# Performance work log

Measured on AMD Instinct MI355X. Metric: run time of the kernel, lower is better.

The kernel has to match this reference:

```python
import jax, jax.numpy as jnp
import numpy as np

D, H, WIN, TEMP = 512, 8, 2, 1.0
DH = D // H
SCALE = DH ** -0.5
SHIFT = WIN // 2


def _ln(x, g, b):
    m = jnp.mean(x, -1, keepdims=True)
    v = jnp.mean(jnp.square(x - m), -1, keepdims=True)
    return (x - m) * jax.lax.rsqrt(v + 1e-5) * g + b


def _win_attn(q, k, v):
    a = jax.nn.softmax(jnp.einsum('nhqd,nhkd->nhqk', q * SCALE, k) / TEMP, axis=-1)
    return jnp.einsum('nhqk,nhkd->nhqd', a, v)


def _self_block(x, p):
    qkv_w, qkv_b, proj_w, proj_b, n1g, n1b, n2g, n2b = p
    b, t, d = x.shape
    sc = x
    xw = _ln(x, n1g, n1b).reshape(b * t // WIN, WIN, d)  # window partition
    qkv = (xw @ qkv_w + qkv_b).reshape(-1, WIN, 3, H, DH).transpose(2, 0, 3, 1, 4)
    o = _win_attn(qkv[0], qkv[1], qkv[2])
    o = o.transpose(0, 2, 1, 3).reshape(-1, WIN, d) @ proj_w + proj_b
    return _ln(o.reshape(b, t, d) + sc, n2g, n2b)  # window reverse + residual


def _self_tf(x, p):
    x = _self_block(x, p)
    x = jnp.roll(x, -SHIFT, axis=1)   # sequence_shift
    x = _self_block(x, p)
    return jnp.roll(x, SHIFT, axis=1)  # sequence_inverse_shift


def _cross_block(x, y, p):
    q_w, q_b, kv_w, kv_b, proj_w, proj_b, n1g, n1b, n2g, n2b = p
    b, t, d = x.shape
    sc = x
    xw = _ln(x, n1g, n1b).reshape(-1, WIN, d)
    yw = _ln(y, n1g, n1b).reshape(-1, WIN, d)  # shared pre_norm, as in source
    q = (xw @ q_w + q_b).reshape(-1, WIN, H, DH).transpose(0, 2, 1, 3)
    kv = (yw @ kv_w + kv_b).reshape(-1, WIN, 2, H, DH).transpose(2, 0, 3, 1, 4)
    o = _win_attn(q, kv[0], kv[1])
    o = o.transpose(0, 2, 1, 3).reshape(-1, WIN, d) @ proj_w + proj_b
    return _ln(o.reshape(b, t, d) + sc, n2g, n2b)


def _cross_tf(x, y, p):
    x = _cross_block(x, y, p)
    x = jnp.roll(x, -SHIFT, axis=1)
    x = _cross_block(x, jnp.roll(y, -SHIFT, axis=1), p)
    return jnp.roll(x, SHIFT, axis=1)


def setup_inputs() -> dict:
    key = jax.random.key(0)
    ks = iter(jax.random.split(key, 40))
    B, T = 16, 4096
    d = {
        'x': jax.random.normal(next(ks), (B, T, D), jnp.float32),
        'y': jax.random.normal(next(ks), (B, T, D), jnp.float32),
    }

    def w(shape):
        return jax.random.normal(next(ks), shape, jnp.float32) * 0.02

    for m in ('wa', 'wv'):  # within-modal audio / video
        d[m + '_qkv_w'] = w((D, 3 * D)); d[m + '_qkv_b'] = jnp.zeros((3 * D,), jnp.float32)
        d[m + '_proj_w'] = w((D, D));    d[m + '_proj_b'] = jnp.zeros((D,), jnp.float32)
        d[m + '_n1_g'] = jnp.ones((D,), jnp.float32); d[m + '_n1_b'] = jnp.zeros((D,), jnp.float32)
        d[m + '_n2_g'] = jnp.ones((D,), jnp.float32); d[m + '_n2_b'] = jnp.zeros((D,), jnp.float32)
    # shared cross-modal transformer
    d['cm_q_w'] = w((D, D));      d['cm_q_b'] = jnp.zeros((D,), jnp.float32)
    d['cm_kv_w'] = w((D, 2 * D)); d['cm_kv_b'] = jnp.zeros((2 * D,), jnp.float32)
    d['cm_proj_w'] = w((D, D));   d['cm_proj_b'] = jnp.zeros((D,), jnp.float32)
    d['cm_n1_g'] = jnp.ones((D,), jnp.float32); d['cm_n1_b'] = jnp.zeros((D,), jnp.float32)
    d['cm_n2_g'] = jnp.ones((D,), jnp.float32); d['cm_n2_b'] = jnp.zeros((D,), jnp.float32)
    return d


def reference(x, y,
              wa_qkv_w, wa_qkv_b, wa_proj_w, wa_proj_b, wa_n1_g, wa_n1_b, wa_n2_g, wa_n2_b,
              wv_qkv_w, wv_qkv_b, wv_proj_w, wv_proj_b, wv_n1_g, wv_n1_b, wv_n2_g, wv_n2_b,
              cm_q_w, cm_q_b, cm_kv_w, cm_kv_b, cm_proj_w, cm_proj_b, cm_n1_g, cm_n1_b, cm_n2_g, cm_n2_b):
    pa = (wa_qkv_w, wa_qkv_b, wa_proj_w, wa_proj_b, wa_n1_g, wa_n1_b, wa_n2_g, wa_n2_b)
    pv = (wv_qkv_w, wv_qkv_b, wv_proj_w, wv_proj_b, wv_n1_g, wv_n1_b, wv_n2_g, wv_n2_b)
    pc = (cm_q_w, cm_q_b, cm_kv_w, cm_kv_b, cm_proj_w, cm_proj_b, cm_n1_g, cm_n1_b, cm_n2_g, cm_n2_b)
    # args.s1_attn == 'all' path
    x = _self_tf(x, pa)
    y = _self_tf(y, pv)
    xc = _cross_tf(x, y, pc)
    yc = _cross_tf(y, x, pc)
    return jnp.stack([x + xc, y + yc])  # (2, B, T, D)
```

## Files before the change

### kernel.cpp

```cpp
#include <hip/hip_runtime.h>

typedef unsigned short u16;
typedef unsigned int u32;
typedef __attribute__((ext_vector_type(8))) short short8;
typedef __attribute__((ext_vector_type(4))) short short4v;
typedef __attribute__((ext_vector_type(4))) float f32x4;

#define D_MODEL 512
#define NH 8
#define TSEQ 4096
#define NB 16
#define NROWS (NB*TSEQ)
#define QK_SCALE 0.125f
#define KDIM 512
#define NKI (KDIM/32)

__device__ __forceinline__ float b2f(u16 u){
    union { float f; unsigned int i; } v; v.i = ((unsigned int)u) << 16; return v.f;
}
__device__ __forceinline__ u16 f2b(float f){
    union { float f; unsigned int i; } v; v.f = f;
    unsigned int r = v.i + 0x7FFFu + ((v.i >> 16) & 1u);
    return (u16)(r >> 16);
}

__device__ __forceinline__ void async_copy16(u16* lds, const u16* g){
    __builtin_amdgcn_global_load_lds(
        (const __attribute__((address_space(1))) u32*)g,
        (__attribute__((address_space(3))) u32*)lds, 16, 0, 0);
}

__global__ void wconv_kernel(const float* __restrict__ W, u16* __restrict__ Wt, int K, int N){
    int idx = blockIdx.x * 256 + threadIdx.x;
    if (idx >= K * N) return;
    int n = idx / K;
    int k = idx - n * K;
    Wt[idx] = f2b(W[(size_t)k * N + n]);
}

__global__ __launch_bounds__(256) void ln_kernel(
    const float* __restrict__ X, const float* __restrict__ g,
    const float* __restrict__ b, u16* __restrict__ out)
{
    int row  = blockIdx.x * 4 + (threadIdx.x >> 6);
    int lane = threadIdx.x & 63;
    size_t base = (size_t)row * D_MODEL + lane * 8;
    float4 x0 = *(const float4*)(X + base);
    float4 x1 = *(const float4*)(X + base + 4);
    float t[8] = {x0.x,x0.y,x0.z,x0.w,x1.x,x1.y,x1.z,x1.w};
    float s = 0.f, ss = 0.f;
    #pragma unroll
    for (int j = 0; j < 8; j++){ s += t[j]; ss += t[j]*t[j]; }
    #pragma unroll
    for (int m = 1; m < 64; m <<= 1){ s += __shfl_xor(s, m); ss += __shfl_xor(ss, m); }
    float mean = s * (1.f/D_MODEL);
    float var  = ss * (1.f/D_MODEL) - mean*mean;
    float rst  = rsqrtf(var + 1e-5f);
    float4 g0 = *(const float4*)(g + lane*8);
    float4 g1 = *(const float4*)(g + lane*8 + 4);
    float4 c0 = *(const float4*)(b + lane*8);
    float4 c1 = *(const float4*)(b + lane*8 + 4);
    float gv[8] = {g0.x,g0.y,g0.z,g0.w,g1.x,g1.y,g1.z,g1.w};
    float bv[8] = {c0.x,c0.y,c0.z,c0.w,c1.x,c1.y,c1.z,c1.w};
    short8 o;
    #pragma unroll
    for (int j = 0; j < 8; j++) o[j] = (short)f2b((t[j]-mean)*rst*gv[j] + bv[j]);
    *(short8*)(out + base) = o;
}

template<int XINBF, int OUTBF>
__global__ __launch_bounds__(256) void resln_kernel(
    const u16* __restrict__ P, const void* __restrict__ Xin,
    const u16* __restrict__ Add,
    const float* __restrict__ g, const float* __restrict__ b,
    void* __restrict__ out,
    u16* __restrict__ lnout, const float* __restrict__ g2, const float* __restrict__ b2)
{
    int row  = blockIdx.x * 4 + (threadIdx.x >> 6);
    int lane = threadIdx.x & 63;
    size_t base = (size_t)row * D_MODEL + lane * 8;
    short8 pv = *(const short8*)(P + base);
    float t[8];
    if constexpr (XINBF){
        short8 xv = *(const short8*)((const u16*)Xin + base);
        #pragma unroll
        for (int j = 0; j < 8; j++) t[j] = b2f((u16)pv[j]) + b2f((u16)xv[j]);
    } else {
        float4 x0 = *(const float4*)((const float*)Xin + base);
        float4 x1 = *(const float4*)((const float*)Xin + base + 4);
        float xr[8] = {x0.x,x0.y,x0.z,x0.w,x1.x,x1.y,x1.z,x1.w};
        #pragma unroll
        for (int j = 0; j < 8; j++) t[j] = b2f((u16)pv[j]) + xr[j];
    }
    float s = 0.f, ss = 0.f;
    #pragma unroll
    for (int j = 0; j < 8; j++){ s += t[j]; ss += t[j]*t[j]; }
    #pragma unroll
    for (int m = 1; m < 64; m <<= 1){ s += __shfl_xor(s, m); ss += __shfl_xor(ss, m); }
    float mean = s * (1.f/D_MODEL);
    float var  = ss * (1.f/D_MODEL) - mean*mean;
    float rst  = rsqrtf(var + 1e-5f);
    float4 g0 = *(const float4*)(g + lane*8);
    float4 g1 = *(const float4*)(g + lane*8 + 4);
    float4 c0 = *(const float4*)(b + lane*8);
    float4 c1 = *(const float4*)(b + lane*8 + 4);
    float gv[8] = {g0.x,g0.y,g0.z,g0.w,g1.x,g1.y,g1.z,g1.w};
    float bv[8] = {c0.x,c0.y,c0.z,c0.w,c1.x,c1.y,c1.z,c1.w};
    float o[8];
    #pragma unroll
    for (int j = 0; j < 8; j++) o[j] = (t[j]-mean)*rst*gv[j] + bv[j];

    if (lnout){
        float s2 = 0.f, ss2 = 0.f;
        #pragma unroll
        for (int j = 0; j < 8; j++){ s2 += o[j]; ss2 += o[j]*o[j]; }
        #pragma unroll
        for (int m = 1; m < 64; m <<= 1){ s2 += __shfl_xor(s2, m); ss2 += __shfl_xor(ss2, m); }
        float mean2 = s2 * (1.f/D_MODEL);
        float var2  = ss2 * (1.f/D_MODEL) - mean2*mean2;
        float rst2  = rsqrtf(var2 + 1e-5f);
        float4 g20 = *(const float4*)(g2 + lane*8);
        float4 g21 = *(const float4*)(g2 + lane*8 + 4);
        float4 b20 = *(const float4*)(b2 + lane*8);
        float4 b21 = *(const float4*)(b2 + lane*8 + 4);
        float g2v[8] = {g20.x,g20.y,g20.z,g20.w,g21.x,g21.y,g21.z,g21.w};
        float b2v[8] = {b20.x,b20.y,b20.z,b20.w,b21.x,b21.y,b21.z,b21.w};
        short8 lo;
        #pragma unroll
        for (int j = 0; j < 8; j++) lo[j] = (short)f2b((o[j]-mean2)*rst2*g2v[j] + b2v[j]);
        *(short8*)(lnout + base) = lo;
    }
    if (Add){
        short8 av = *(const short8*)(Add + base);
        #pragma unroll
        for (int j = 0; j < 8; j++) o[j] += b2f((u16)av[j]);
    }
    if constexpr (OUTBF){
        short8 ov;
        #pragma unroll
        for (int j = 0; j < 8; j++) ov[j] = (short)f2b(o[j]);
        *(short8*)((u16*)out + base) = ov;
    } else {
        float4 r0 = {o[0],o[1],o[2],o[3]};
        float4 r1 = {o[4],o[5],o[6],o[7]};
        *(float4*)((float*)out + base)     = r0;
        *(float4*)((float*)out + base + 4) = r1;
    }
}

__global__ __launch_bounds__(256) void qkvattn_kernel(
    const u16* __restrict__ A, const u16* __restrict__ Wt,
    const float* __restrict__ bias, u16* __restrict__ O, int shift)
{
    __shared__ __align__(16) u16 lds[2][20*512];
    int tid  = threadIdx.x;
    int lane = tid & 63;
    int wid  = tid >> 6;

    int bid  = blockIdx.x;
    int swz  = (bid & 7) * 512 + (bid >> 3);
    int head = swz >> 9;
    int rt   = swz & 511;
    int bt   = rt >> 5;
    int tb   = (rt & 31) * 128;

    f32x4 acc[2][12];
    f32x4 zero = {0.f,0.f,0.f,0.f};
    #pragma unroll
    for (int m = 0; m < 2; m++)
        #pragma unroll
        for (int n = 0; n < 12; n++) acc[m][n] = zero;

    int rr = lane >> 2, kc = (lane & 3) * 8;
    const u16* p[5];
    int cidb = wid * 5;
    #pragma unroll
    for (int q = 0; q < 5; q++){
        int cid = cidb + q;
        if (cid < 8){
            int i   = cid*16 + rr;
            int tok = (tb + shift + i) & (TSEQ-1);
            p[q] = A + ((size_t)bt * TSEQ + tok) * KDIM + kc;
        } else {
            int cb   = cid - 8;
            int wrow = (cb >> 2) * 512 + head*64 + (cb & 3)*16 + rr;
            p[q] = Wt + (size_t)wrow * KDIM + kc;
        }
    }

    int lrow = lane & 15;
    int lk   = (lane >> 4) * 8;
    int aoff = (wid*32 + lrow) * 32 + lk;
    int boff = 8*512 + lrow*32 + lk;

    #pragma unroll
    for (int q = 0; q < 5; q++){ async_copy16(&lds[0][(cidb+q)*512], p[q]); p[q] += 32; }
    asm volatile("s_waitcnt vmcnt(0)" ::: "memory");
    __syncthreads();

    #pragma unroll
    for (int t = 0; t < NKI; t++){
        const u16* cbuf = lds[t & 1];
        u16* nbuf = (u16*)lds[(t & 1) ^ 1];
        if (t < NKI-1){
            #pragma unroll
            for (int q = 0; q < 5; q++){ async_copy16(&nbuf[(cidb+q)*512], p[q]); p[q] += 32; }
        }
        short8 af[2], bf[12];
        #pragma unroll
        for (int m = 0; m < 2; m++) af[m] = *(const short8*)(cbuf + aoff + m*512);
        #pragma unroll
        for (int n = 0; n < 12; n++) bf[n] = *(const short8*)(cbuf + boff + n*512);
        #pragma unroll
        for (int m = 0; m < 2; m++)
            #pragma unroll
            for (int n = 0; n < 12; n++)
                acc[m][n] = __builtin_amdgcn_mfma_f32_16x16x32_bf16(af[m], bf[n], acc[m][n], 0, 0, 0);
        if (t < NKI-1){
            asm volatile("s_waitcnt vmcnt(0)" ::: "memory");
            __syncthreads();
        }
    }

    int g_ = lane >> 4, lc = lane & 15;
    float bq[4], bk[4], bv[4];
    #pragma unroll
    for (int n = 0; n < 4; n++){
        int d = head*64 + n*16 + lc;
        bq[n] = bias[d]; bk[n] = bias[512 + d]; bv[n] = bias[1024 + d];
    }
    #pragma unroll
    for (int m = 0; m < 2; m++){
        #pragma unroll
        for (int wnd = 0; wnd < 2; wnd++){
            int ja = 2*wnd, jb = ja + 1;
            float s00=0.f, s01=0.f, s10=0.f, s11=0.f;
            #pragma unroll
            for (int n = 0; n < 4; n++){
                float qa = acc[m][n][ja] + bq[n],  qb = acc[m][n][jb] + bq[n];
                float ka = acc[m][4+n][ja] + bk[n], kb = acc[m][4+n][jb] + bk[n];
                s00 += qa*ka; s01 += qa*kb; s10 += qb*ka; s11 += qb*kb;
            }
            #pragma unroll
            for (int msk = 1; msk < 16; msk <<= 1){
                s00 += __shfl_xor(s00, msk); s01 += __shfl_xor(s01, msk);
                s10 += __shfl_xor(s10, msk); s11 += __shfl_xor(s11, msk);
            }
            s00 *= QK_SCALE; s01 *= QK_SCALE; s10 *= QK_SCALE; s11 *= QK_SCALE;
            float m0 = fmaxf(s00, s01), m1 = fmaxf(s10, s11);
            float e00 = expf(s00-m0), e01 = expf(s01-m0);
            float e10 = expf(s10-m1), e11 = expf(s11-m1);
            float ia = 1.f/(e00+e01), ib = 1.f/(e10+e11);
            float a00 = e00*ia, a01 = e01*ia, a10 = e10*ib, a11 = e11*ib;
            int ra = wid*32 + m*16 + 4*g_ + ja;
            int ta = (tb + shift + ra) & (TSEQ-1);
            size_t growa = (size_t)bt * TSEQ + ta;
            size_t growb = (size_t)bt * TSEQ + ((ta + 1) & (TSEQ-1));
            #pragma unroll
            for (int n = 0; n < 4; n++){
                float va = acc[m][8+n][ja] + bv[n], vb = acc[m][8+n][jb] + bv[n];
                int col = head*64 + n*16 + lc;
                O[growa * D_MODEL + col] = f2b(a00*va + a01*vb);
                O[growb * D_MODEL + col] = f2b(a10*va + a11*vb);
            }
        }
    }
}

#define AOFc(buf,h) (((buf)*2+(h))*8192)
#define BOFc(buf,h) (32768 + ((buf)*2+(h))*8192)

__global__ __launch_bounds__(512, 2) void gemm256_kernel(
    const u16* __restrict__ A, const u16* __restrict__ Wt,
    const float* __restrict__ bias, u16* __restrict__ C, int N, int nN)
{
    __shared__ __align__(16) u16 sh[65536];
    u16* sh_ = (u16*)sh;
    const int tid = threadIdx.x, lane = tid & 63, wid = tid >> 6;
    const int wm = wid >> 2, wn = wid & 3;
    const int cpx = (int)gridDim.x >> 3;
    const int swz = ((int)blockIdx.x & 7) * cpx + ((int)blockIdx.x >> 3);
    const int row0 = (swz / nN) * 256;
    const int col0 = (swz % nN) * 256;

    f32x4 acc[8][4];
    f32x4 zero = {0.f,0.f,0.f,0.f};
    #pragma unroll
    for (int m = 0; m < 8; m++)
        #pragma unroll
        for (int n = 0; n < 4; n++) acc[m][n] = zero;

    const int lrow = lane & 15, khi = lane >> 4;
    const int swx   = (lrow & 4) << 2;
    const int kcol0 = (khi*8) ^ swx;
    const int kcol1 = (32 + khi*8) ^ swx;
    const int aR0 = AOFc(0, wm) , aR1 = AOFc(1, wm);
    const int bh  = wn >> 1;
    const int bR0 = BOFc(0, bh), bR1 = BOFc(1, bh);
    const int abase = lrow*64;
    const int bbase = (wn & 1)*4096 + lrow*64;

    const u16* Ag = A  + (size_t)row0 * KDIM;
    const u16* Bg = Wt + (size_t)col0 * KDIM;
    const int csrc = ((lane & 7) * 8) ^ (((lane >> 3) & 4) << 2);
    const int srow = wid*16 + (lane >> 3);

    short8 af[4][2], bf[4][2];

    #define STG(dstOff, gp) { \
        const u16* s1_ = (gp) + (size_t)srow*KDIM + csrc; \
        u16* d1_ = sh_ + (dstOff) + wid*1024; \
        async_copy16(d1_, s1_); \
        async_copy16(d1_ + 512, s1_ + (size_t)8*KDIM); }
    #define RDA(bufR, h) { \
        const u16* p_ = sh_ + (bufR) + abase; \
        _Pragma("unroll") \
        for (int i_ = 0; i_ < 4; i_++){ \
            af[i_][0] = *(const short8*)(p_ + ((h)*4+i_)*1024 + kcol0); \
            af[i_][1] = *(const short8*)(p_ + ((h)*4+i_)*1024 + kcol1); } }
    #define RDB(bufR, nh) { \
        const u16* p_ = sh_ + (bufR) + bbase; \
        _Pragma("unroll") \
        for (int j_ = 0; j_ < 2; j_++){ \
            bf[(nh)*2+j_][0] = *(const short8*)(p_ + ((nh)*2+j_)*1024 + kcol0); \
            bf[(nh)*2+j_][1] = *(const short8*)(p_ + ((nh)*2+j_)*1024 + kcol1); } }
    #define MM(mh, nh) { \
        __builtin_amdgcn_s_setprio(1); \
        _Pragma("unroll") \
        for (int m_ = 0; m_ < 4; m_++) \
            _Pragma("unroll") \
            for (int n_ = 0; n_ < 2; n_++){ \
                acc[(mh)*4+m_][(nh)*2+n_] = __builtin_amdgcn_mfma_f32_16x16x32_bf16(af[m_][0], bf[(nh)*2+n_][0], acc[(mh)*4+m_][(nh)*2+n_], 0,0,0); \
                acc[(mh)*4+m_][(nh)*2+n_] = __builtin_amdgcn_mfma_f32_16x16x32_bf16(af[m_][1], bf[(nh)*2+n_][1], acc[(mh)*4+m_][(nh)*2+n_], 0,0,0); } \
        __builtin_amdgcn_s_setprio(0); }
    #define BAR() { asm volatile("" ::: "memory"); __builtin_amdgcn_s_barrier(); asm volatile("" ::: "memory"); }
    #define VMW4() asm volatile("s_waitcnt vmcnt(4)" ::: "memory")
    #define VMW0() asm volatile("s_waitcnt vmcnt(0)" ::: "memory")

    STG(BOFc(0,0), Bg);
    STG(BOFc(0,1), Bg + (size_t)128*KDIM);
    STG(AOFc(0,0), Ag);
    STG(AOFc(0,1), Ag + (size_t)128*KDIM);
    STG(BOFc(1,0), Bg + 64);
    STG(BOFc(1,1), Bg + (size_t)128*KDIM + 64);
    VMW4();
    BAR();

    #pragma unroll
    for (int i = 0; i < 4; i++){
        RDA(aR0, 0); RDB(bR0, 0);
        STG(AOFc(1,0), Ag + (2*i+1)*64);
        BAR(); MM(0,0); BAR();

        RDB(bR0, 1);
        STG(AOFc(1,1), Ag + (size_t)128*KDIM + (2*i+1)*64);
        BAR(); MM(0,1); BAR();

        RDA(aR0, 1);
        if (i < 3) STG(BOFc(0,0), Bg + (2*i+2)*64);
        BAR(); MM(1,0); BAR();

        if (i < 3){ STG(BOFc(0,1), Bg + (size_t)128*KDIM + (2*i+2)*64); VMW4(); }
        else      { VMW0(); }
        BAR(); MM(1,1); BAR();

        RDA(aR1, 0); RDB(bR1, 0);
        if (i < 3) STG(AOFc(0,0), Ag + (2*i+2)*64);
        BAR(); MM(0,0); BAR();

        RDB(bR1, 1);
        if (i < 3) STG(AOFc(0,1), Ag + (size_t)128*KDIM + (2*i+2)*64);
        BAR(); MM(0,1); BAR();

        RDA(aR1, 1);
        if (i < 3) STG(BOFc(1,0), Bg + (2*i+3)*64);
        BAR(); MM(1,0); BAR();

        if (i < 3){ STG(BOFc(1,1), Bg + (size_t)128*KDIM + (2*i+3)*64); VMW4(); }
        BAR(); MM(1,1); BAR();
    }

    int g_ = lane >> 4, lc = lane & 15;
    #pragma unroll
    for (int n = 0; n < 4; n++){
        int c = col0 + wn*64 + n*16 + lc;
        float bvv = bias[c];
        #pragma unroll
        for (int m = 0; m < 8; m++){
            int r = row0 + wm*128 + m*16 + 4*g_;
            f32x4 v = acc[m][n];
            C[(size_t)(r+0) * N + c] = f2b(v[0] + bvv);
            C[(size_t)(r+1) * N + c] = f2b(v[1] + bvv);
            C[(size_t)(r+2) * N + c] = f2b(v[2] + bvv);
            C[(size_t)(r+3) * N + c] = f2b(v[3] + bvv);
        }
    }
    #undef STG
    #undef RDA
    #undef RDB
    #undef MM
    #undef BAR
    #undef VMW4
    #undef VMW0
}

__global__ __launch_bounds__(256) void attn_cross_kernel(
    const u16* __restrict__ Q, const u16* __restrict__ KV,
    u16* __restrict__ O, int shift)
{
    int tsk  = blockIdx.x * 4 + (threadIdx.x >> 6);
    int lane = threadIdx.x & 63;
    int w  = tsk >> 1;
    int hb = tsk & 1;
    int bt = w >> 11;
    int wt = w & 2047;
    int t0 = (2*wt + shift) & (TSEQ - 1);
    int t1 = (t0 + 1) & (TSEQ - 1);
    size_t g0 = (size_t)bt * TSEQ + t0;
    size_t g1 = (size_t)bt * TSEQ + t1;
    int col = hb*256 + lane*4;
    short4v q0 = *(const short4v*)(Q  + g0*512  + col);
    short4v q1 = *(const short4v*)(Q  + g1*512  + col);
    short4v k0 = *(const short4v*)(KV + g0*1024 + col);
    short4v k1 = *(const short4v*)(KV + g1*1024 + col);
    short4v v0 = *(const short4v*)(KV + g0*1024 + 512 + col);
    short4v v1 = *(const short4v*)(KV + g1*1024 + 512 + col);
    float s00=0.f, s01=0.f, s10=0.f, s11=0.f;
    float v0f[4], v1f[4];
    #pragma unroll
    for (int j = 0; j < 4; j++){
        float qa = b2f((u16)q0[j]), qb = b2f((u16)q1[j]);
        float ka = b2f((u16)k0[j]), kb = b2f((u16)k1[j]);
        v0f[j] = b2f((u16)v0[j]); v1f[j] = b2f((u16)v1[j]);
        s00 += qa*ka; s01 += qa*kb; s10 += qb*ka; s11 += qb*kb;
    }
    #pragma unroll
    for (int m = 1; m < 16; m <<= 1){
        s00 += __shfl_xor(s00, m); s01 += __shfl_xor(s01, m);
        s10 += __shfl_xor(s10, m); s11 += __shfl_xor(s11, m);
    }
    s00 *= QK_SCALE; s01 *= QK_SCALE; s10 *= QK_SCALE; s11 *= QK_SCALE;
    float m0 = fmaxf(s00, s01), m1 = fmaxf(s10, s11);
    float e00 = expf(s00 - m0), e01 = expf(s01 - m0);
    float e10 = expf(s10 - m1), e11 = expf(s11 - m1);
    float ia = 1.f/(e00 + e01), ib = 1.f/(e10 + e11);
    float a00 = e00*ia, a01 = e01*ia, a10 = e10*ib, a11 = e11*ib;
    short4v o0, o1;
    #pragma unroll
    for (int j = 0; j < 4; j++){
        o0[j] = (short)f2b(a00*v0f[j] + a01*v1f[j]);
        o1[j] = (short)f2b(a10*v0f[j] + a11*v1f[j]);
    }
    *(short4v*)(O + g0*512 + col) = o0;
    *(short4v*)(O + g1*512 + col) = o1;
}

extern "C" void kernel_launch(void* const* d_in, const int* in_sizes, int n_in,
                              void* d_out, int out_size, void* d_ws, size_t ws_size,
                              hipStream_t stream)
{
    const float* x = (const float*)d_in[0];
    const float* y = (const float*)d_in[1];
    const float* wa_qkv_w = (const float*)d_in[2];  const float* wa_qkv_b = (const float*)d_in[3];
    const float* wa_proj_w= (const float*)d_in[4];  const float* wa_proj_b= (const float*)d_in[5];
    const float* wa_n1g   = (const float*)d_in[6];  const float* wa_n1b   = (const float*)d_in[7];
    const float* wa_n2g   = (const float*)d_in[8];  const float* wa_n2b   = (const float*)d_in[9];
    const float* wv_qkv_w = (const float*)d_in[10]; const float* wv_qkv_b = (const float*)d_in[11];
    const float* wv_proj_w= (const float*)d_in[12]; const float* wv_proj_b= (const float*)d_in[13];
    const float* wv_n1g   = (const float*)d_in[14]; const float* wv_n1b   = (const float*)d_in[15];
    const float* wv_n2g   = (const float*)d_in[16]; const float* wv_n2b   = (const float*)d_in[17];
    const float* cm_q_w   = (const float*)d_in[18]; const float* cm_q_b   = (const float*)d_in[19];
    const float* cm_kv_w  = (const float*)d_in[20]; const float* cm_kv_b  = (const float*)d_in[21];
    const float* cm_proj_w= (const float*)d_in[22]; const float* cm_proj_b= (const float*)d_in[23];
    const float* cm_n1g   = (const float*)d_in[24]; const float* cm_n1b   = (const float*)d_in[25];
    const float* cm_n2g   = (const float*)d_in[26]; const float* cm_n2b   = (const float*)d_in[27];

    char* ws = (char*)d_ws;
    const size_t SZ_B16 = (size_t)NROWS * D_MODEL * 2;
    u16* F1b = (u16*)(ws);
    u16* XFb = (u16*)(ws + 1*SZ_B16);
    u16* YFb = (u16*)(ws + 2*SZ_B16);
    u16* XN  = (u16*)(ws + 3*SZ_B16);
    u16* CN  = (u16*)(ws + 4*SZ_B16);
    u16* XLN = (u16*)(ws + 5*SZ_B16);
    u16* YLN = (u16*)(ws + 6*SZ_B16);
    u16* O   = (u16*)(ws + 7*SZ_B16);
    u16* KVb = (u16*)(ws + 8*SZ_B16);
    u16* WB  = (u16*)(ws + 10*SZ_B16);

    u16* PB = KVb;

    u16* wa_qkv_t  = WB;
    u16* wa_proj_t = wa_qkv_t  + 1536*512;
    u16* wv_qkv_t  = wa_proj_t + 512*512;
    u16* wv_proj_t = wv_qkv_t  + 1536*512;
    u16* cm_q_t    = wv_proj_t + 512*512;
    u16* cm_kv_t   = cm_q_t    + 512*512;
    u16* cm_proj_t = cm_kv_t   + 1024*512;

    auto conv = [&](const float* W, u16* Wt, int K, int N){
        int total = K * N;
        wconv_kernel<<<(total + 255) / 256, 256, 0, stream>>>(W, Wt, K, N);
    };
    conv(wa_qkv_w,  wa_qkv_t,  512, 1536);
    conv(wa_proj_w, wa_proj_t, 512, 512);
    conv(wv_qkv_w,  wv_qkv_t,  512, 1536);
    conv(wv_proj_w, wv_proj_t, 512, 512);
    conv(cm_q_w,    cm_q_t,    512, 512);
    conv(cm_kv_w,   cm_kv_t,   512, 1024);
    conv(cm_proj_w, cm_proj_t, 512, 512);

    const int lnGrid   = NROWS / 4;
    const int attnGrid = NROWS / 2 * 2 / 4;
    const int qaGrid   = (NROWS / 128) * NH;

    auto gemm = [&](const u16* Ain, const u16* Wt, const float* bias, u16* Cout, int N){
        int nN = N / 256;
        gemm256_kernel<<<(NROWS/256) * nN, 512, 0, stream>>>(Ain, Wt, bias, Cout, N, nN);
    };

    auto self_chain = [&](const float* in, u16* outFb, u16* outLN,
                          const u16* qkvT, const float* qkv_b,
                          const u16* projT, const float* proj_b,
                          const float* n1g, const float* n1b,
                          const float* n2g, const float* n2b){
        ln_kernel<<<lnGrid, 256, 0, stream>>>(in, n1g, n1b, XN);
        qkvattn_kernel<<<qaGrid, 256, 0, stream>>>(XN, qkvT, qkv_b, O, 0);
        gemm(O, projT, proj_b, PB, 512);
        resln_kernel<0,1><<<lnGrid, 256, 0, stream>>>(PB, in, nullptr, n2g, n2b, F1b, XN, n1g, n1b);
        qkvattn_kernel<<<qaGrid, 256, 0, stream>>>(XN, qkvT, qkv_b, O, 1);
        gemm(O, projT, proj_b, PB, 512);
        resln_kernel<1,1><<<lnGrid, 256, 0, stream>>>(PB, F1b, nullptr, n2g, n2b, outFb, outLN, cm_n1g, cm_n1b);
    };

    self_chain(x, XFb, XLN, wa_qkv_t, wa_qkv_b, wa_proj_t, wa_proj_b, wa_n1g, wa_n1b, wa_n2g, wa_n2b);
    self_chain(y, YFb, YLN, wv_qkv_t, wv_qkv_b, wv_proj_t, wv_proj_b, wv_n1g, wv_n1b, wv_n2g, wv_n2b);

    float* out0 = (float*)d_out;
    float* out1 = out0 + (size_t)NROWS * D_MODEL;

    auto cross_chain = [&](const u16* qLN, const u16* kvLN, const u16* resFb, float* outF){
        gemm(kvLN, cm_kv_t, cm_kv_b, KVb, 1024);
        gemm(qLN,  cm_q_t,  cm_q_b,  XN,  512);
        attn_cross_kernel<<<attnGrid, 256, 0, stream>>>(XN, KVb, O, 0);
        gemm(O, cm_proj_t, cm_proj_b, XN, 512);
        resln_kernel<1,1><<<lnGrid, 256, 0, stream>>>(XN, resFb, nullptr, cm_n2g, cm_n2b, F1b, CN, cm_n1g, cm_n1b);
        gemm(CN, cm_q_t, cm_q_b, XN, 512);
        attn_cross_kernel<<<attnGrid, 256, 0, stream>>>(XN, KVb, O, 1);
        gemm(O, cm_proj_t, cm_proj_b, XN, 512);
        resln_kernel<1,0><<<lnGrid, 256, 0, stream>>>(XN, F1b, resFb, cm_n2g, cm_n2b, outF, nullptr, nullptr, nullptr);
    };

    cross_chain(XLN, YLN, XFb, out0);
    cross_chain(YLN, XLN, YFb, out1);
}
```

Measured before the change: 2.144 ms.

## Batch x and y streams into single launches over concatenated rows

```diff
diff --git a/kernel.cpp b/kernel.cpp
--- a/kernel.cpp
+++ b/kernel.cpp
@@ -11,6 +11,7 @@
 #define TSEQ 4096
 #define NB 16
 #define NROWS (NB*TSEQ)
+#define M2 (2*NROWS)
 #define QK_SCALE 0.125f
 #define KDIM 512
 #define NKI (KDIM/32)
@@ -30,12 +31,25 @@
         (__attribute__((address_space(3))) u32*)lds, 16, 0, 0);
 }
 
-__global__ void wconv_kernel(const float* __restrict__ W, u16* __restrict__ Wt, int K, int N){
+__global__ void wconv_all_kernel(
+    const float* __restrict__ s0, const float* __restrict__ s1,
+    const float* __restrict__ s2, const float* __restrict__ s3,
+    const float* __restrict__ s4, const float* __restrict__ s5,
+    const float* __restrict__ s6, u16* __restrict__ dst)
+{
     int idx = blockIdx.x * 256 + threadIdx.x;
-    if (idx >= K * N) return;
-    int n = idx / K;
-    int k = idx - n * K;
-    Wt[idx] = f2b(W[(size_t)k * N + n]);
+    int off = idx;
+    const float* W; int N;
+    if      (off < 786432)                    { W = s0; N = 1536; }
+    else if ((off -= 786432) < 262144)        { W = s1; N = 512;  }
+    else if ((off -= 262144) < 786432)        { W = s2; N = 1536; }
+    else if ((off -= 786432) < 262144)        { W = s3; N = 512;  }
+    else if ((off -= 262144) < 262144)        { W = s4; N = 512;  }
+    else if ((off -= 262144) < 524288)        { W = s5; N = 1024; }
+    else    { off -= 524288;                    W = s6; N = 512;  }
+    int n = off >> 9;
+    int k = off & 511;
+    dst[idx] = f2b(W[(size_t)k * N + n]);
 }
 
 __global__ __launch_bounds__(256) void ln_kernel(
@@ -149,8 +163,9 @@
 }
 
 __global__ __launch_bounds__(256) void qkvattn_kernel(
-    const u16* __restrict__ A, const u16* __restrict__ Wt,
-    const float* __restrict__ bias, u16* __restrict__ O, int shift)
+    const u16* __restrict__ A, const u16* __restrict__ Wt0, const u16* __restrict__ Wt1,
+    const float* __restrict__ bias0, const float* __restrict__ bias1,
+    u16* __restrict__ O, int shift)
 {
     __shared__ __align__(16) u16 lds[2][20*512];
     int tid  = threadIdx.x;
@@ -158,11 +173,18 @@
     int wid  = tid >> 6;
 
     int bid  = blockIdx.x;
-    int swz  = (bid & 7) * 512 + (bid >> 3);
-    int head = swz >> 9;
-    int rt   = swz & 511;
-    int bt   = rt >> 5;
-    int tb   = (rt & 31) * 128;
+    int swz  = (bid & 7) * 1024 + (bid >> 3);
+    int head = swz >> 10;
+    int rt   = swz & 1023;
+    int half = rt >> 9;
+    int hrt  = rt & 511;
+    int bt   = hrt >> 5;
+    int tb   = (hrt & 31) * 128;
+
+    const u16*  Wt   = half ? Wt1   : Wt0;
+    const float* bias = half ? bias1 : bias0;
+    const u16* Ab = A + (size_t)half * NROWS * D_MODEL;
+    u16*       Ob = O + (size_t)half * NROWS * D_MODEL;
 
     f32x4 acc[2][12];
     f32x4 zero = {0.f,0.f,0.f,0.f};
@@ -180,7 +202,7 @@
         if (cid < 8){
             int i   = cid*16 + rr;
             int tok = (tb + shift + i) & (TSEQ-1);
-            p[q] = A + ((size_t)bt * TSEQ + tok) * KDIM + kc;
+            p[q] = Ab + ((size_t)bt * TSEQ + tok) * KDIM + kc;
         } else {
             int cb   = cid - 8;
             int wrow = (cb >> 2) * 512 + head*64 + (cb & 3)*16 + rr;
@@ -260,8 +282,8 @@
             for (int n = 0; n < 4; n++){
                 float va = acc[m][8+n][ja] + bv[n], vb = acc[m][8+n][jb] + bv[n];
                 int col = head*64 + n*16 + lc;
-                O[growa * D_MODEL + col] = f2b(a00*va + a01*vb);
-                O[growb * D_MODEL + col] = f2b(a10*va + a11*vb);
+                Ob[growa * D_MODEL + col] = f2b(a00*va + a01*vb);
+                Ob[growb * D_MODEL + col] = f2b(a10*va + a11*vb);
             }
         }
     }
@@ -271,8 +293,10 @@
 #define BOFc(buf,h) (32768 + ((buf)*2+(h))*8192)
 
 __global__ __launch_bounds__(512, 2) void gemm256_kernel(
-    const u16* __restrict__ A, const u16* __restrict__ Wt,
-    const float* __restrict__ bias, u16* __restrict__ C, int N, int nN)
+    const u16* __restrict__ A,
+    const u16* __restrict__ Wt0, const u16* __restrict__ Wt1,
+    const float* __restrict__ bias0, const float* __restrict__ bias1,
+    u16* __restrict__ C, int N, int nN, int halfM)
 {
     __shared__ __align__(16) u16 sh[65536];
     u16* sh_ = (u16*)sh;
@@ -282,6 +306,9 @@
     const int swz = ((int)blockIdx.x & 7) * cpx + ((int)blockIdx.x >> 3);
     const int row0 = (swz / nN) * 256;
     const int col0 = (swz % nN) * 256;
+
+    const u16*  Wt   = (row0 >= halfM) ? Wt1   : Wt0;
+    const float* bias = (row0 >= halfM) ? bias1 : bias0;
 
     f32x4 acc[8][4];
     f32x4 zero = {0.f,0.f,0.f,0.f};
@@ -418,13 +445,15 @@
     int t1 = (t0 + 1) & (TSEQ - 1);
     size_t g0 = (size_t)bt * TSEQ + t0;
     size_t g1 = (size_t)bt * TSEQ + t1;
+    size_t kg0 = g0 ^ (size_t)NROWS;
+    size_t kg1 = g1 ^ (size_t)NROWS;
     int col = hb*256 + lane*4;
     short4v q0 = *(const short4v*)(Q  + g0*512  + col);
     short4v q1 = *(const short4v*)(Q  + g1*512  + col);
-    short4v k0 = *(const short4v*)(KV + g0*1024 + col);
-    short4v k1 = *(const short4v*)(KV + g1*1024 + col);
-    short4v v0 = *(const short4v*)(KV + g0*1024 + 512 + col);
-    short4v v1 = *(const short4v*)(KV + g1*1024 + 512 + col);
+    short4v k0 = *(const short4v*)(KV + kg0*1024 + col);
+    short4v k1 = *(const short4v*)(KV + kg1*1024 + col);
+    short4v v0 = *(const short4v*)(KV + kg0*1024 + 512 + col);
+    short4v v1 = *(const short4v*)(KV + kg1*1024 + 512 + col);
     float s00=0.f, s01=0.f, s10=0.f, s11=0.f;
     float v0f[4], v1f[4];
     #pragma unroll
@@ -476,19 +505,18 @@
     const float* cm_n2g   = (const float*)d_in[26]; const float* cm_n2b   = (const float*)d_in[27];
 
     char* ws = (char*)d_ws;
-    const size_t SZ_B16 = (size_t)NROWS * D_MODEL * 2;
+    const size_t HALF = (size_t)NROWS * D_MODEL;
+    const size_t SZ2  = (size_t)M2 * D_MODEL * 2;
     u16* F1b = (u16*)(ws);
-    u16* XFb = (u16*)(ws + 1*SZ_B16);
-    u16* YFb = (u16*)(ws + 2*SZ_B16);
-    u16* XN  = (u16*)(ws + 3*SZ_B16);
-    u16* CN  = (u16*)(ws + 4*SZ_B16);
-    u16* XLN = (u16*)(ws + 5*SZ_B16);
-    u16* YLN = (u16*)(ws + 6*SZ_B16);
-    u16* O   = (u16*)(ws + 7*SZ_B16);
-    u16* KVb = (u16*)(ws + 8*SZ_B16);
-    u16* WB  = (u16*)(ws + 10*SZ_B16);
-
-    u16* PB = KVb;
+    u16* SFb = (u16*)(ws + 1*SZ2);
+    u16* SLN = (u16*)(ws + 2*SZ2);
+    u16* XN  = (u16*)(ws + 3*SZ2);
+    u16* O   = (u16*)(ws + 4*SZ2);
+    u16* KVA = (u16*)(ws + 5*SZ2);
+    u16* WB  = (u16*)(ws + 7*SZ2);
+
+    u16* CN = SLN;
+    u16* PB = KVA;
 
     u16* wa_qkv_t  = WB;
     u16* wa_proj_t = wa_qkv_t  + 1536*512;
@@ -498,59 +526,43 @@
     u16* cm_kv_t   = cm_q_t    + 512*512;
     u16* cm_proj_t = cm_kv_t   + 1024*512;
 
-    auto conv = [&](const float* W, u16* Wt, int K, int N){
-        int total = K * N;
-        wconv_kernel<<<(total + 255) / 256, 256, 0, stream>>>(W, Wt, K, N);
+    wconv_all_kernel<<<12288, 256, 0, stream>>>(
+        wa_qkv_w, wa_proj_w, wv_qkv_w, wv_proj_w, cm_q_w, cm_kv_w, cm_proj_w, wa_qkv_t);
+
+    const int lnGridH   = NROWS / 4;
+    const int rlGrid2   = M2 / 4;
+    const int attnGrid2 = M2 / 2 * 2 / 4;
+    const int qaGrid2   = (M2 / 128) * NH;
+
+    auto gemm = [&](const u16* Ain, const u16* W0, const u16* W1,
+                    const float* b0, const float* b1, u16* Cout, int N, int halfM){
+        int nN = N / 256;
+        gemm256_kernel<<<(M2/256) * nN, 512, 0, stream>>>(Ain, W0, W1, b0, b1, Cout, N, nN, halfM);
     };
-    conv(wa_qkv_w,  wa_qkv_t,  512, 1536);
-    conv(wa_proj_w, wa_proj_t, 512, 512);
-    conv(wv_qkv_w,  wv_qkv_t,  512, 1536);
-    conv(wv_proj_w, wv_proj_t, 512, 512);
-    conv(cm_q_w,    cm_q_t,    512, 512);
-    conv(cm_kv_w,   cm_kv_t,   512, 1024);
-    conv(cm_proj_w, cm_proj_t, 512, 512);
-
-    const int lnGrid   = NROWS / 4;
-    const int attnGrid = NROWS / 2 * 2 / 4;
-    const int qaGrid   = (NROWS / 128) * NH;
-
-    auto gemm = [&](const u16* Ain, const u16* Wt, const float* bias, u16* Cout, int N){
-        int nN = N / 256;
-        gemm256_kernel<<<(NROWS/256) * nN, 512, 0, stream>>>(Ain, Wt, bias, Cout, N, nN);
-    };
-
-    auto self_chain = [&](const float* in, u16* outFb, u16* outLN,
-                          const u16* qkvT, const float* qkv_b,
-                          const u16* projT, const float* proj_b,
-                          const float* n1g, const float* n1b,
-                          const float* n2g, const float* n2b){
-        ln_kernel<<<lnGrid, 256, 0, stream>>>(in, n1g, n1b, XN);
-        qkvattn_kernel<<<qaGrid, 256, 0, stream>>>(XN, qkvT, qkv_b, O, 0);
-        gemm(O, projT, proj_b, PB, 512);
-        resln_kernel<0,1><<<lnGrid, 256, 0, stream>>>(PB, in, nullptr, n2g, n2b, F1b, XN, n1g, n1b);
-        qkvattn_kernel<<<qaGrid, 256, 0, stream>>>(XN, qkvT, qkv_b, O, 1);
-        gemm(O, projT, proj_b, PB, 512);
-        resln_kernel<1,1><<<lnGrid, 256, 0, stream>>>(PB, F1b, nullptr, n2g, n2b, outFb, outLN, cm_n1g, cm_n1b);
-    };
-
-    self_chain(x, XFb, XLN, wa_qkv_t, wa_qkv_b, wa_proj_t, wa_proj_b, wa_n1g, wa_n1b, wa_n2g, wa_n2b);
-    self_chain(y, YFb, YLN, wv_qkv_t, wv_qkv_b, wv_proj_t, wv_proj_b, wv_n1g, wv_n1b, wv_n2g, wv_n2b);
-
-    float* out0 = (float*)d_out;
-    float* out1 = out0 + (size_t)NROWS * D_MODEL;
-
-    auto cross_chain = [&](const u16* qLN, const u16* kvLN, const u16* resFb, float* outF){
-        gemm(kvLN, cm_kv_t, cm_kv_b, KVb, 1024);
-        gemm(qLN,  cm_q_t,  cm_q_b,  XN,  512);
-        attn_cross_kernel<<<attnGrid, 256, 0, stream>>>(XN, KVb, O, 0);
-        gemm(O, cm_proj_t, cm_proj_b, XN, 512);
-        resln_kernel<1,1><<<lnGrid, 256, 0, stream>>>(XN, resFb, nullptr, cm_n2g, cm_n2b, F1b, CN, cm_n1g, cm_n1b);
-        gemm(CN, cm_q_t, cm_q_b, XN, 512);
-        attn_cross_kernel<<<attnGrid, 256, 0, stream>>>(XN, KVb, O, 1);
-        gemm(O, cm_proj_t, cm_proj_b, XN, 512);
-        resln_kernel<1,0><<<lnGrid, 256, 0, stream>>>(XN, F1b, resFb, cm_n2g, cm_n2b, outF, nullptr, nullptr, nullptr);
-    };
-
-    cross_chain(XLN, YLN, XFb, out0);
-    cross_chain(YLN, XLN, YFb, out1);
-}
+
+    ln_kernel<<<lnGridH, 256, 0, stream>>>(x, wa_n1g, wa_n1b, XN);
+    ln_kernel<<<lnGridH, 256, 0, stream>>>(y, wv_n1g, wv_n1b, XN + HALF);
+
+    qkvattn_kernel<<<qaGrid2, 256, 0, stream>>>(XN, wa_qkv_t, wv_qkv_t, wa_qkv_b, wv_qkv_b, O, 0);
+    gemm(O, wa_proj_t, wv_proj_t, wa_proj_b, wv_proj_b, PB, 512, NROWS);
+    resln_kernel<0,1><<<lnGridH, 256, 0, stream>>>(PB,        x, nullptr, wa_n2g, wa_n2b, F1b,        XN,        wa_n1g, wa_n1b);
+    resln_kernel<0,1><<<lnGridH, 256, 0, stream>>>(PB + HALF, y, nullptr, wv_n2g, wv_n2b, F1b + HALF, XN + HALF, wv_n1g, wv_n1b);
+
+    qkvattn_kernel<<<qaGrid2, 256, 0, stream>>>(XN, wa_qkv_t, wv_qkv_t, wa_qkv_b, wv_qkv_b, O, 1);
+    gemm(O, wa_proj_t, wv_proj_t, wa_proj_b, wv_proj_b, PB, 512, NROWS);
+    resln_kernel<1,1><<<lnGridH, 256, 0, stream>>>(PB,        F1b,        nullptr, wa_n2g, wa_n2b, SFb,        SLN,        cm_n1g, cm_n1b);
+    resln_kernel<1,1><<<lnGridH, 256, 0, stream>>>(PB + HALF, F1b + HALF, nullptr, wv_n2g, wv_n2b, SFb + HALF, SLN + HALF, cm_n1g, cm_n1b);
+
+    float* outF = (float*)d_out;
+
+    gemm(SLN, cm_kv_t, cm_kv_t, cm_kv_b, cm_kv_b, KVA, 1024, M2);
+    gemm(SLN, cm_q_t,  cm_q_t,  cm_q_b,  cm_q_b,  XN,  512,  M2);
+    attn_cross_kernel<<<attnGrid2, 256, 0, stream>>>(XN, KVA, O, 0);
+    gemm(O, cm_proj_t, cm_proj_t, cm_proj_b, cm_proj_b, XN, 512, M2);
+    resln_kernel<1,1><<<rlGrid2, 256, 0, stream>>>(XN, SFb, nullptr, cm_n2g, cm_n2b, F1b, CN, cm_n1g, cm_n1b);
+
+    gemm(CN, cm_q_t, cm_q_t, cm_q_b, cm_q_b, XN, 512, M2);
+    attn_cross_kernel<<<attnGrid2, 256, 0, stream>>>(XN, KVA, O, 1);
+    gemm(O, cm_proj_t, cm_proj_t, cm_proj_b, cm_proj_b, XN, 512, M2);
+    resln_kernel<1,0><<<rlGrid2, 256, 0, stream>>>(XN, F1b, SFb, cm_n2g, cm_n2b, outF, nullptr, nullptr, nullptr);
+}
```

Measured after the change: 2.510 ms. 17.1% more time.
